# Optimization experiments

Hardware: AMD Instinct MI355X
Metric: run time of the kernel (lower is better)

Reference implementation:

```python
import jax, jax.numpy as jnp
import numpy as np

N_NODES = 50000
N_EDGES = 800000
D_IN = 128
D_OUT = 128
ALPHA = 0.2  # LeakyReLU negative slope


def setup_inputs() -> dict:
    key = jax.random.key(0)
    k1, k2, k3, k4 = jax.random.split(key, 4)
    x = jax.random.normal(k1, (N_NODES, D_IN), dtype=jnp.float32)
    W = jax.random.normal(k2, (D_IN, D_OUT), dtype=jnp.float32) * (1.414 / np.sqrt(D_IN))
    a = jax.random.normal(k3, (2 * D_OUT, 1), dtype=jnp.float32) * 0.1
    edge_index = jax.random.randint(k4, (2, N_EDGES), 0, N_NODES, dtype=jnp.int64)
    return {"x": x, "W": W, "a": a, "edge_index": edge_index}


def reference(x, W, a, edge_index):
    # h: (N, D_OUT)
    h = x @ W
    src, dst = edge_index[0], edge_index[1]
    # e_i = leakyrelu([h[src]; h[dst]] @ a) == leakyrelu((h@a1)[src] + (h@a2)[dst])
    a1 = a[:D_OUT, 0]
    a2 = a[D_OUT:, 0]
    s1 = h @ a1  # (N,)
    s2 = h @ a2  # (N,)
    e = jax.nn.leaky_relu(s1[src] + s2[dst], negative_slope=ALPHA)  # (E,)
    # Global softmax over all edges (faithful to F.softmax(edge_e, dim=0))
    attention = jax.nn.softmax(e)  # (E,)
    # output[dst] += attention * h[src]  (scatter-add)
    msgs = attention[:, None] * h[src]  # (E, D_OUT)
    output = jax.ops.segment_sum(msgs, dst, num_segments=N_NODES)
    return output
```

## Files before the change

### kernel.cpp

```cpp
#include <hip/hip_runtime.h>
#include <hip/hip_bf16.h>

#define N_NODES 50000
#define N_EDGES 800000
#define D 128
#define ALPHA 0.2f
#define NEG_INF -1e30f

#define KB_BLOCKS 1024
#define NSCAN_BLOCKS ((N_NODES + 255) / 256)
#define LDS_STRIDE 272

typedef __attribute__((ext_vector_type(8))) short short8;
typedef __attribute__((ext_vector_type(4))) float floatx4;

__device__ __forceinline__ unsigned int f2bf(float v)
{
    __hip_bfloat16 b = __float2bfloat16(v);
    return (unsigned int)*reinterpret_cast<unsigned short*>(&b);
}
__device__ __forceinline__ float bf_lo(unsigned int u)
{
    return __uint_as_float(u << 16);
}
__device__ __forceinline__ float bf_hi(unsigned int u)
{
    return __uint_as_float(u & 0xFFFF0000u);
}

__global__ __launch_bounds__(256) void k_wprep(
    const float* __restrict__ W, const float* __restrict__ a,
    float* __restrict__ w12)
{
    const int t = threadIdx.x;
    const int i = t & 127;
    const int which = t >> 7;
    const float* av = a + which * D;
    float acc = 0.f;
    #pragma unroll 8
    for (int j = 0; j < D; ++j)
        acc += W[(size_t)i * D + j] * av[j];
    w12[which * D + i] = acc;
}

__global__ __launch_bounds__(256) void k_fused(
    const float* __restrict__ x, const float* __restrict__ W,
    const float* __restrict__ w12, const int* __restrict__ ei,
    unsigned short* __restrict__ hb, float* __restrict__ s1,
    float* __restrict__ s2, int* __restrict__ deg)
{
    __shared__ unsigned char lds[16 * LDS_STRIDE];
    const int t = threadIdx.x;
    const int rowbase = blockIdx.x * 16;

    const int r = t >> 4;
    const int c = t & 15;
    const float* xp = x + (size_t)(rowbase + r) * D + c * 8;
    const float4 v0 = *(const float4*)(xp);
    const float4 v1 = *(const float4*)(xp + 4);

    const int lane = t & 63;
    const int wv = t >> 6;
    const int q = lane >> 4;
    const int nIdx = lane & 15;
    const int n0 = wv * 32;
    short8 B[2][4];
    #pragma unroll
    for (int kt = 0; kt < 4; ++kt) {
        short8 be, bo;
        #pragma unroll
        for (int j = 0; j < 8; ++j) {
            const float* wp = W + (size_t)(kt * 32 + q * 8 + j) * D + n0 + 2 * nIdx;
            be[j] = (short)f2bf(wp[0]);
            bo[j] = (short)f2bf(wp[1]);
        }
        B[0][kt] = be;
        B[1][kt] = bo;
    }

    {
        const float* w1 = w12 + c * 8;
        const float* w2 = w12 + D + c * 8;
        float p1 = v0.x * w1[0] + v0.y * w1[1] + v0.z * w1[2] + v0.w * w1[3]
                 + v1.x * w1[4] + v1.y * w1[5] + v1.z * w1[6] + v1.w * w1[7];
        float p2 = v0.x * w2[0] + v0.y * w2[1] + v0.z * w2[2] + v0.w * w2[3]
                 + v1.x * w2[4] + v1.y * w2[5] + v1.z * w2[6] + v1.w * w2[7];
        #pragma unroll
        for (int mask = 8; mask >= 1; mask >>= 1) {
            p1 += __shfl_xor(p1, mask);
            p2 += __shfl_xor(p2, mask);
        }
        if (c == 0) { s1[rowbase + r] = p1; s2[rowbase + r] = p2; }

        uint4 pk;
        pk.x = f2bf(v0.x) | (f2bf(v0.y) << 16);
        pk.y = f2bf(v0.z) | (f2bf(v0.w) << 16);
        pk.z = f2bf(v1.x) | (f2bf(v1.y) << 16);
        pk.w = f2bf(v1.z) | (f2bf(v1.w) << 16);
        *(uint4*)(lds + r * LDS_STRIDE + c * 16) = pk;
    }
    __syncthreads();

    const unsigned char* ab = lds + nIdx * LDS_STRIDE + q * 16;
    const short8 A0 = *(const short8*)(ab);
    const short8 A1 = *(const short8*)(ab + 64);
    const short8 A2 = *(const short8*)(ab + 128);
    const short8 A3 = *(const short8*)(ab + 192);

    floatx4 acc0 = {0.f, 0.f, 0.f, 0.f};
    floatx4 acc1 = {0.f, 0.f, 0.f, 0.f};
    acc0 = __builtin_amdgcn_mfma_f32_16x16x32_bf16(A0, B[0][0], acc0, 0, 0, 0);
    acc1 = __builtin_amdgcn_mfma_f32_16x16x32_bf16(A0, B[1][0], acc1, 0, 0, 0);
    acc0 = __builtin_amdgcn_mfma_f32_16x16x32_bf16(A1, B[0][1], acc0, 0, 0, 0);
    acc1 = __builtin_amdgcn_mfma_f32_16x16x32_bf16(A1, B[1][1], acc1, 0, 0, 0);
    acc0 = __builtin_amdgcn_mfma_f32_16x16x32_bf16(A2, B[0][2], acc0, 0, 0, 0);
    acc1 = __builtin_amdgcn_mfma_f32_16x16x32_bf16(A2, B[1][2], acc1, 0, 0, 0);
    acc0 = __builtin_amdgcn_mfma_f32_16x16x32_bf16(A3, B[0][3], acc0, 0, 0, 0);
    acc1 = __builtin_amdgcn_mfma_f32_16x16x32_bf16(A3, B[1][3], acc1, 0, 0, 0);

    #pragma unroll
    for (int i = 0; i < 4; ++i) {
        const int row = rowbase + q * 4 + i;
        const unsigned int pk = f2bf(acc0[i]) | (f2bf(acc1[i]) << 16);
        *(unsigned int*)(hb + (size_t)row * D + n0 + 2 * nIdx) = pk;
    }

    const int e = blockIdx.x * 256 + t;
    atomicAdd(&deg[ei[N_EDGES + e]], 1);
}

__device__ __forceinline__ void online_combine(float& m, float& s,
                                               float om, float os)
{
    float nm = fmaxf(m, om);
    s = s * __expf(m - nm) + os * __expf(om - nm);
    m = nm;
}

__global__ __launch_bounds__(256) void k_scan_a(
    const int* __restrict__ deg, int* __restrict__ partials)
{
    const int i = blockIdx.x * 256 + threadIdx.x;
    int v = (i < N_NODES) ? deg[i] : 0;
    #pragma unroll
    for (int off = 32; off >= 1; off >>= 1) v += __shfl_down(v, off);
    __shared__ int ws[4];
    if ((threadIdx.x & 63) == 0) ws[threadIdx.x >> 6] = v;
    __syncthreads();
    if (threadIdx.x == 0)
        partials[blockIdx.x] = ws[0] + ws[1] + ws[2] + ws[3];
}

__global__ __launch_bounds__(256) void k_scan_b(
    const int* __restrict__ partials, int* __restrict__ partialOffs,
    int* __restrict__ offs)
{
    __shared__ int sc[256];
    const int t = threadIdx.x;
    int v = (t < NSCAN_BLOCKS) ? partials[t] : 0;
    sc[t] = v;
    __syncthreads();
    #pragma unroll
    for (int off = 1; off < 256; off <<= 1) {
        int u = (t >= off) ? sc[t - off] : 0;
        __syncthreads();
        sc[t] += u;
        __syncthreads();
    }
    if (t < NSCAN_BLOCKS) partialOffs[t] = sc[t] - v;
    if (t == 255) offs[N_NODES] = sc[255];
}

__global__ __launch_bounds__(256) void k_scan_c(
    const int* __restrict__ deg, const int* __restrict__ partialOffs,
    int* __restrict__ offs, int* __restrict__ cursor)
{
    __shared__ int sc[256];
    const int t = threadIdx.x;
    const int i = blockIdx.x * 256 + t;
    const int v = (i < N_NODES) ? deg[i] : 0;
    sc[t] = v;
    __syncthreads();
    #pragma unroll
    for (int off = 1; off < 256; off <<= 1) {
        int u = (t >= off) ? sc[t - off] : 0;
        __syncthreads();
        sc[t] += u;
        __syncthreads();
    }
    if (i < N_NODES) {
        const int o = partialOffs[blockIdx.x] + sc[t] - v;
        offs[i] = o;
        cursor[i] = o;
    }
}

__global__ __launch_bounds__(256) void k_bucket(
    const int* __restrict__ ei, const float* __restrict__ s1,
    const float* __restrict__ s2, int* __restrict__ cursor,
    int2* __restrict__ csr, float* __restrict__ bm, float* __restrict__ bs)
{
    const int* src = ei;
    const int* dst = ei + N_EDGES;
    float m = NEG_INF, s = 0.f;
    for (int e = blockIdx.x * blockDim.x + threadIdx.x; e < N_EDGES;
         e += blockDim.x * gridDim.x) {
        const int sN = src[e];
        const int dN = dst[e];
        float v = s1[sN] + s2[dN];
        v = v > 0.f ? v : ALPHA * v;
        const int pos = atomicAdd(&cursor[dN], 1);
        csr[pos] = make_int2(sN, __float_as_int(v));
        float nm = fmaxf(m, v);
        s = s * __expf(m - nm) + __expf(v - nm);
        m = nm;
    }
    #pragma unroll
    for (int off = 32; off >= 1; off >>= 1) {
        float om = __shfl_down(m, off);
        float os = __shfl_down(s, off);
        online_combine(m, s, om, os);
    }
    __shared__ float rm[4], rs[4];
    const int wid = threadIdx.x >> 6;
    if ((threadIdx.x & 63) == 0) { rm[wid] = m; rs[wid] = s; }
    __syncthreads();
    if (threadIdx.x == 0) {
        #pragma unroll
        for (int w = 1; w < 4; ++w) online_combine(m, s, rm[w], rs[w]);
        bm[blockIdx.x] = m;
        bs[blockIdx.x] = s;
    }
}

__global__ __launch_bounds__(256) void k_reduce_mz(
    const float* __restrict__ bm, const float* __restrict__ bs,
    float* __restrict__ MZ)
{
    float m = NEG_INF, s = 0.f;
    for (int i = threadIdx.x; i < KB_BLOCKS; i += 256)
        online_combine(m, s, bm[i], bs[i]);
    #pragma unroll
    for (int off = 32; off >= 1; off >>= 1) {
        float om = __shfl_down(m, off);
        float os = __shfl_down(s, off);
        online_combine(m, s, om, os);
    }
    __shared__ float rm[4], rs[4];
    const int wid = threadIdx.x >> 6;
    if ((threadIdx.x & 63) == 0) { rm[wid] = m; rs[wid] = s; }
    __syncthreads();
    if (threadIdx.x == 0) {
        #pragma unroll
        for (int w = 1; w < 4; ++w) online_combine(m, s, rm[w], rs[w]);
        MZ[0] = m;
        MZ[1] = s;
    }
}

__global__ __launch_bounds__(256) void k_gather(
    const int2* __restrict__ csr, const int* __restrict__ offs,
    const unsigned short* __restrict__ hb, const float* __restrict__ MZ,
    float* __restrict__ out)
{
    const int node = (blockIdx.x * blockDim.x + threadIdx.x) >> 6;
    if (node >= N_NODES) return;
    const int lane = threadIdx.x & 63;
    const float M = MZ[0];
    const float invZ = 1.0f / MZ[1];
    const int beg = offs[node];
    const int end = offs[node + 1];

    float a0 = 0.f, a1 = 0.f, b0 = 0.f, b1 = 0.f;
    float c0 = 0.f, c1 = 0.f, d0 = 0.f, d1 = 0.f;

    for (int cb = beg; cb < end; cb += 64) {
        const int n = min(64, end - cb);
        int2 p = make_int2(0, __float_as_int(NEG_INF));
        if (cb + lane < end) p = csr[cb + lane];
        const int srcl = p.x;
        const float attl = __expf(__int_as_float(p.y) - M) * invZ;

        int j = 0;
        for (; j + 3 < n; j += 4) {
            const int i0 = __shfl(srcl, j);
            const int i1 = __shfl(srcl, j + 1);
            const int i2 = __shfl(srcl, j + 2);
            const int i3 = __shfl(srcl, j + 3);
            const float w0 = __shfl(attl, j);
            const float w1 = __shfl(attl, j + 1);
            const float w2 = __shfl(attl, j + 2);
            const float w3 = __shfl(attl, j + 3);
            const unsigned int u0 =
                *(const unsigned int*)(hb + (size_t)i0 * D + lane * 2);
            const unsigned int u1 =
                *(const unsigned int*)(hb + (size_t)i1 * D + lane * 2);
            const unsigned int u2 =
                *(const unsigned int*)(hb + (size_t)i2 * D + lane * 2);
            const unsigned int u3 =
                *(const unsigned int*)(hb + (size_t)i3 * D + lane * 2);
            a0 += w0 * bf_lo(u0); a1 += w0 * bf_hi(u0);
            b0 += w1 * bf_lo(u1); b1 += w1 * bf_hi(u1);
            c0 += w2 * bf_lo(u2); c1 += w2 * bf_hi(u2);
            d0 += w3 * bf_lo(u3); d1 += w3 * bf_hi(u3);
        }
        for (; j < n; ++j) {
            const int i0 = __shfl(srcl, j);
            const float w0 = __shfl(attl, j);
            const unsigned int u0 =
                *(const unsigned int*)(hb + (size_t)i0 * D + lane * 2);
            a0 += w0 * bf_lo(u0); a1 += w0 * bf_hi(u0);
        }
    }
    float2 r;
    r.x = (a0 + b0) + (c0 + d0);
    r.y = (a1 + b1) + (c1 + d1);
    *(float2*)(out + (size_t)node * D + lane * 2) = r;
}

extern "C" void kernel_launch(void* const* d_in, const int* in_sizes, int n_in,
                              void* d_out, int out_size, void* d_ws, size_t ws_size,
                              hipStream_t stream)
{
    const float* x = (const float*)d_in[0];
    const float* W = (const float*)d_in[1];
    const float* a = (const float*)d_in[2];
    const int* ei = (const int*)d_in[3];
    float* out = (float*)d_out;

    char* wsb = (char*)d_ws;
    int2* csr = (int2*)wsb;
    unsigned short* hb = (unsigned short*)(wsb + (size_t)N_EDGES * 8);
    float* s1     = (float*)((char*)hb + (size_t)N_NODES * D * 2);
    float* s2     = s1 + N_NODES;
    int*   deg    = (int*)(s2 + N_NODES);
    int*   offs   = deg + N_NODES;
    int*   cursor = offs + N_NODES + 1;
    int*   partials    = cursor + N_NODES;
    int*   partialOffs = partials + NSCAN_BLOCKS;
    float* w12    = (float*)(partialOffs + NSCAN_BLOCKS);
    float* bm     = w12 + 2 * D;
    float* bs     = bm + KB_BLOCKS;
    float* MZ     = bs + KB_BLOCKS;

    hipMemsetAsync(deg, 0, N_NODES * sizeof(int), stream);

    k_wprep<<<1, 256, 0, stream>>>(W, a, w12);
    k_fused<<<N_NODES / 16, 256, 0, stream>>>(x, W, w12, ei, hb, s1, s2, deg);
    k_scan_a<<<NSCAN_BLOCKS, 256, 0, stream>>>(deg, partials);
    k_scan_b<<<1, 256, 0, stream>>>(partials, partialOffs, offs);
    k_scan_c<<<NSCAN_BLOCKS, 256, 0, stream>>>(deg, partialOffs, offs, cursor);
    k_bucket<<<KB_BLOCKS, 256, 0, stream>>>(ei, s1, s2, cursor, csr, bm, bs);
    k_reduce_mz<<<1, 256, 0, stream>>>(bm, bs, MZ);
    k_gather<<<(N_NODES * 64 + 255) / 256, 256, 0, stream>>>(
        csr, offs, hb, MZ, out);
}
```

Measured before the change: 207.6 us.

## Record per-edge rank during degree count to build CSR without cursor atomics

The degree-counting atomic in the fused kernel now stores its return value as a per-edge rank, so the bucket pass writes each edge to offs[dst]+rank with no second atomic pass and no cursor array. The CSR shrinks to 4-byte source indices, and the gather kernel recomputes the LeakyReLU score from s1/s2 instead of reading a stored score. The bucket kernel becomes one edge per thread with 3125 blocks. This trades an extra rank array write/read and a random s1 gather in the gather kernel for removing the contended cursor atomics and halving CSR traffic.

After: 186.8 us. -10.0%, faster.

```diff
diff --git a/kernel.cpp b/kernel.cpp
--- a/kernel.cpp
+++ b/kernel.cpp
@@ -7,7 +7,7 @@
 #define ALPHA 0.2f
 #define NEG_INF -1e30f
 
-#define KB_BLOCKS 1024
+#define KB_BLOCKS 3125
 #define NSCAN_BLOCKS ((N_NODES + 255) / 256)
 #define LDS_STRIDE 272
 
@@ -47,7 +47,7 @@
     const float* __restrict__ x, const float* __restrict__ W,
     const float* __restrict__ w12, const int* __restrict__ ei,
     unsigned short* __restrict__ hb, float* __restrict__ s1,
-    float* __restrict__ s2, int* __restrict__ deg)
+    float* __restrict__ s2, int* __restrict__ deg, int* __restrict__ rank)
 {
     __shared__ unsigned char lds[16 * LDS_STRIDE];
     const int t = threadIdx.x;
@@ -126,7 +126,7 @@
     }
 
     const int e = blockIdx.x * 256 + t;
-    atomicAdd(&deg[ei[N_EDGES + e]], 1);
+    rank[e] = atomicAdd(&deg[ei[N_EDGES + e]], 1);
 }
 
 __device__ __forceinline__ void online_combine(float& m, float& s,
@@ -173,7 +173,7 @@
 
 __global__ __launch_bounds__(256) void k_scan_c(
     const int* __restrict__ deg, const int* __restrict__ partialOffs,
-    int* __restrict__ offs, int* __restrict__ cursor)
+    int* __restrict__ offs)
 {
     __shared__ int sc[256];
     const int t = threadIdx.x;
@@ -188,33 +188,25 @@
         sc[t] += u;
         __syncthreads();
     }
-    if (i < N_NODES) {
-        const int o = partialOffs[blockIdx.x] + sc[t] - v;
-        offs[i] = o;
-        cursor[i] = o;
-    }
+    if (i < N_NODES)
+        offs[i] = partialOffs[blockIdx.x] + sc[t] - v;
 }
 
 __global__ __launch_bounds__(256) void k_bucket(
     const int* __restrict__ ei, const float* __restrict__ s1,
-    const float* __restrict__ s2, int* __restrict__ cursor,
-    int2* __restrict__ csr, float* __restrict__ bm, float* __restrict__ bs)
-{
-    const int* src = ei;
-    const int* dst = ei + N_EDGES;
-    float m = NEG_INF, s = 0.f;
-    for (int e = blockIdx.x * blockDim.x + threadIdx.x; e < N_EDGES;
-         e += blockDim.x * gridDim.x) {
-        const int sN = src[e];
-        const int dN = dst[e];
-        float v = s1[sN] + s2[dN];
-        v = v > 0.f ? v : ALPHA * v;
-        const int pos = atomicAdd(&cursor[dN], 1);
-        csr[pos] = make_int2(sN, __float_as_int(v));
-        float nm = fmaxf(m, v);
-        s = s * __expf(m - nm) + __expf(v - nm);
-        m = nm;
-    }
+    const float* __restrict__ s2, const int* __restrict__ offs,
+    const int* __restrict__ rank, unsigned int* __restrict__ csr,
+    float* __restrict__ bm, float* __restrict__ bs)
+{
+    const int e = blockIdx.x * 256 + threadIdx.x;
+    const int sN = ei[e];
+    const int dN = ei[N_EDGES + e];
+    csr[offs[dN] + rank[e]] = (unsigned int)sN;
+
+    float v = s1[sN] + s2[dN];
+    v = v > 0.f ? v : ALPHA * v;
+
+    float m = v, s = 1.f;
     #pragma unroll
     for (int off = 32; off >= 1; off >>= 1) {
         float om = __shfl_down(m, off);
@@ -259,7 +251,8 @@
 }
 
 __global__ __launch_bounds__(256) void k_gather(
-    const int2* __restrict__ csr, const int* __restrict__ offs,
+    const unsigned int* __restrict__ csr, const int* __restrict__ offs,
+    const float* __restrict__ s1, const float* __restrict__ s2,
     const unsigned short* __restrict__ hb, const float* __restrict__ MZ,
     float* __restrict__ out)
 {
@@ -268,6 +261,7 @@
     const int lane = threadIdx.x & 63;
     const float M = MZ[0];
     const float invZ = 1.0f / MZ[1];
+    const float s2n = s2[node];
     const int beg = offs[node];
     const int end = offs[node + 1];
 
@@ -276,10 +270,10 @@
 
     for (int cb = beg; cb < end; cb += 64) {
         const int n = min(64, end - cb);
-        int2 p = make_int2(0, __float_as_int(NEG_INF));
-        if (cb + lane < end) p = csr[cb + lane];
-        const int srcl = p.x;
-        const float attl = __expf(__int_as_float(p.y) - M) * invZ;
+        const int srcl = (cb + lane < end) ? (int)csr[cb + lane] : 0;
+        float v = s1[srcl] + s2n;
+        v = v > 0.f ? v : ALPHA * v;
+        const float attl = __expf(v - M) * invZ;
 
         int j = 0;
         for (; j + 3 < n; j += 4) {
@@ -329,14 +323,14 @@
     float* out = (float*)d_out;
 
     char* wsb = (char*)d_ws;
-    int2* csr = (int2*)wsb;
-    unsigned short* hb = (unsigned short*)(wsb + (size_t)N_EDGES * 8);
-    float* s1     = (float*)((char*)hb + (size_t)N_NODES * D * 2);
+    unsigned int* csr = (unsigned int*)wsb;
+    unsigned short* hb = (unsigned short*)(wsb + (size_t)N_EDGES * 4);
+    int* rank     = (int*)((char*)hb + (size_t)N_NODES * D * 2);
+    float* s1     = (float*)(rank + N_EDGES);
     float* s2     = s1 + N_NODES;
     int*   deg    = (int*)(s2 + N_NODES);
     int*   offs   = deg + N_NODES;
-    int*   cursor = offs + N_NODES + 1;
-    int*   partials    = cursor + N_NODES;
+    int*   partials    = offs + N_NODES + 1;
     int*   partialOffs = partials + NSCAN_BLOCKS;
     float* w12    = (float*)(partialOffs + NSCAN_BLOCKS);
     float* bm     = w12 + 2 * D;
@@ -346,12 +340,14 @@
     hipMemsetAsync(deg, 0, N_NODES * sizeof(int), stream);
 
     k_wprep<<<1, 256, 0, stream>>>(W, a, w12);
-    k_fused<<<N_NODES / 16, 256, 0, stream>>>(x, W, w12, ei, hb, s1, s2, deg);
+    k_fused<<<N_NODES / 16, 256, 0, stream>>>(x, W, w12, ei, hb, s1, s2,
+                                              deg, rank);
     k_scan_a<<<NSCAN_BLOCKS, 256, 0, stream>>>(deg, partials);
     k_scan_b<<<1, 256, 0, stream>>>(partials, partialOffs, offs);
-    k_scan_c<<<NSCAN_BLOCKS, 256, 0, stream>>>(deg, partialOffs, offs, cursor);
-    k_bucket<<<KB_BLOCKS, 256, 0, stream>>>(ei, s1, s2, cursor, csr, bm, bs);
+    k_scan_c<<<NSCAN_BLOCKS, 256, 0, stream>>>(deg, partialOffs, offs);
+    k_bucket<<<KB_BLOCKS, 256, 0, stream>>>(ei, s1, s2, offs, rank, csr,
+                                            bm, bs);
     k_reduce_mz<<<1, 256, 0, stream>>>(bm, bs, MZ);
     k_gather<<<(N_NODES * 64 + 255) / 256, 256, 0, stream>>>(
-        csr, offs, hb, MZ, out);
-}
+        csr, offs, s1, s2, hb, MZ, out);
+}
```
